# Optimization experiments

Measured on AMD Instinct MI355X. Metric: run time of the kernel, lower is better.

Reference implementation:

```python
import jax, jax.numpy as jnp
import numpy as np
import math

H = 8
D_MODEL = 512
D_K = D_MODEL // H
DIM_G = 64
WAVE_LEN = 1000.0


def box_relational_embedding(f_g):
    # f_g: [B, N, 4] -> [B, N, N, 64] trigonometric geometry embedding
    x_min, y_min, x_max, y_max = jnp.split(f_g, 4, axis=-1)  # each [B,N,1]
    cx = (x_min + x_max) * 0.5
    cy = (y_min + y_max) * 0.5
    w = x_max - x_min + 1.0
    h = y_max - y_min + 1.0
    # pairwise deltas: [B,N,1] vs [B,1,N] -> [B,N,N]
    cx_t = jnp.swapaxes(cx, 1, 2)  # [B,1,N]
    cy_t = jnp.swapaxes(cy, 1, 2)
    w_t = jnp.swapaxes(w, 1, 2)
    h_t = jnp.swapaxes(h, 1, 2)
    delta_x = jnp.log(jnp.maximum(jnp.abs((cx - cx_t) / w), 0.001))
    delta_y = jnp.log(jnp.maximum(jnp.abs((cy - cy_t) / h), 0.001))
    delta_w = jnp.log(w / w_t)
    delta_h = jnp.log(h / h_t)
    position_mat = jnp.stack([delta_x, delta_y, delta_w, delta_h], axis=-1)  # [B,N,N,4]
    feat_range = jnp.arange(DIM_G // 8, dtype=position_mat.dtype) / (DIM_G / 8)
    dim_mat = 1.0 / jnp.power(jnp.asarray(WAVE_LEN, position_mat.dtype), feat_range)  # [8]
    mul_mat = (100.0 * position_mat)[..., None] * dim_mat  # [B,N,N,4,8]
    B, N = position_mat.shape[0], position_mat.shape[1]
    mul_mat = mul_mat.reshape(B, N, N, -1)  # [B,N,N,32]
    return jnp.concatenate([jnp.sin(mul_mat), jnp.cos(mul_mat)], axis=-1)  # [B,N,N,64]


def setup_inputs() -> dict:
    key = jax.random.key(0)
    ks = jax.random.split(key, 16)
    B, N = 16, 256
    scale = 1.0 / math.sqrt(D_MODEL)
    inp = {
        'input_query': jax.random.normal(ks[0], (B, N, D_MODEL), jnp.float32),
        'input_key': jax.random.normal(ks[1], (B, N, D_MODEL), jnp.float32),
        'input_value': jax.random.normal(ks[2], (B, N, D_MODEL), jnp.float32),
        'input_box': jax.random.uniform(ks[3], (B, N, 4), jnp.float32),
        'mask': jnp.ones((B, N), jnp.int32),
        # projection weights stored as [d_in, d_out] (x @ W + b)
        'Wq': jax.random.normal(ks[4], (D_MODEL, D_MODEL), jnp.float32) * scale,
        'bq': jnp.zeros((D_MODEL,), jnp.float32),
        'Wk': jax.random.normal(ks[5], (D_MODEL, D_MODEL), jnp.float32) * scale,
        'bk': jnp.zeros((D_MODEL,), jnp.float32),
        'Wv': jax.random.normal(ks[6], (D_MODEL, D_MODEL), jnp.float32) * scale,
        'bv': jnp.zeros((D_MODEL,), jnp.float32),
        'Wo': jax.random.normal(ks[7], (D_MODEL, D_MODEL), jnp.float32) * scale,
        'bo': jnp.zeros((D_MODEL,), jnp.float32),
        # 8 geometric-bias heads: Linear(64 -> 1) each, stacked -> [H, 64], [H]
        'WG_w': jax.random.normal(ks[8], (H, DIM_G), jnp.float32) * (1.0 / math.sqrt(DIM_G)),
        'WG_b': jnp.zeros((H,), jnp.float32),
    }
    return inp


def reference(input_query, input_key, input_value, input_box, mask,
              Wq, bq, Wk, bk, Wv, bv, Wo, bo, WG_w, WG_b):
    B, N, _ = input_query.shape

    def proj(x, W, b):  # [B,N,D] -> [B,H,N,d_k]
        return (x @ W + b).reshape(B, N, H, D_K).transpose(0, 2, 1, 3)

    q = proj(input_query, Wq, bq)
    k = proj(input_key, Wk, bk)
    v = proj(input_value, Wv, bv)

    geo = box_relational_embedding(input_box)  # [B,N,N,64]
    # per-head geometric weights, ReLU'd: [B,H,N,N]
    w_g = jax.nn.relu(jnp.einsum('bnmg,hg->bhnm', geo, WG_w) + WG_b[None, :, None, None])

    scaled_dot = jnp.einsum('bhqd,bhkd->bhqk', q, k) / np.sqrt(D_K).astype(q.dtype)
    # mask: [B,N] keys -> [B,1,1,N], broadcast over heads and queries
    scaled_dot = jnp.where(mask[:, None, None, :] == 0, jnp.asarray(-1e9, scaled_dot.dtype), scaled_dot)
    w_mn = jax.nn.softmax(jnp.log(jnp.maximum(w_g, 1e-6)) + scaled_dot, axis=-1)
    # dropout is identity in eval mode
    out = jnp.einsum('bhqk,bhkd->bhqd', w_mn, v)  # [B,H,N,d_k]
    out = out.transpose(0, 2, 1, 3).reshape(B, N, H * D_K)
    return out @ Wo + bo
```

## Files before the change

### kernel.cpp

```cpp
#include <hip/hip_runtime.h>
#include <hip/hip_fp16.h>
#include <math.h>

#define Bv   16
#define Nv   256
#define Dv   512
#define Hv   8
#define MNv  4096

typedef __attribute__((ext_vector_type(8))) short bf16x8;
typedef __attribute__((ext_vector_type(4))) float f32x4;
typedef __fp16 fp16x8 __attribute__((ext_vector_type(8)));
typedef __fp16 fp16x2 __attribute__((ext_vector_type(2)));

__device__ __forceinline__ unsigned short f2bf(float f) {
    unsigned u = __float_as_uint(f);
    u = u + 0x7FFFu + ((u >> 16) & 1u);
    return (unsigned short)(u >> 16);
}
__device__ __forceinline__ void gload_lds16(const void* g, void* l) {
    __builtin_amdgcn_global_load_lds(
        (const __attribute__((address_space(1))) unsigned int*)g,
        (__attribute__((address_space(3))) unsigned int*)l, 16, 0, 0);
}

__device__ __forceinline__ void fast_sincos(float x, float* s, float* c) {
    const float rev = x * 0.15915494309189535f;
    const float fr  = rev - floorf(rev);
    *s = __builtin_amdgcn_sinf(fr);
    *c = __builtin_amdgcn_cosf(fr);
}
__device__ __forceinline__ float fast_log(float x) {
    return __builtin_amdgcn_logf(x) * 0.6931471805599453f;
}
__device__ __forceinline__ float fast_exp(float x) {
    return __builtin_amdgcn_exp2f(x * 1.4426950408889634f);
}

__global__ __launch_bounds__(256) void mega1_kernel(
    const float* __restrict__ box, const int* __restrict__ mask,
    const float* __restrict__ WGw, const float* __restrict__ WGb,
    __half* __restrict__ LB,
    const float* __restrict__ xq, const float* __restrict__ xk,
    const float* __restrict__ xv, unsigned short* __restrict__ Ab,
    const float* __restrict__ Wq, const float* __restrict__ Wk,
    const float* __restrict__ Wv, const float* __restrict__ Wo,
    const float* __restrict__ bq, const float* __restrict__ bk,
    const float* __restrict__ bv, const float* __restrict__ bo,
    unsigned short* __restrict__ Wt, float* __restrict__ biasStack)
{
    __shared__ __align__(16) char smraw[64 * 65 * 4];
    const int bid = blockIdx.x;
    const int t = threadIdx.x;

    if (bid < 4096) {
        unsigned short (*Lst)[264] = (unsigned short (*)[264])smraw;
        const int q = bid & 255;
        const int b = bid >> 8;
        const int w = t >> 6, lane = t & 63;
        const int n = lane & 15;
        const int quad = lane >> 4;

        const float4 bq_ = *(const float4*)(box + (b * Nv + q) * 4);
        const float cxq = (bq_.x + bq_.z) * 0.5f;
        const float cyq = (bq_.y + bq_.w) * 0.5f;
        const float wq  = bq_.z - bq_.x + 1.0f;
        const float hq  = bq_.w - bq_.y + 1.0f;

        union F16x8 { fp16x8 v; fp16x2 p[4]; };
        F16x8 Bs_, Bc_;
        Bs_.v = (fp16x8){}; Bc_.v = (fp16x8){};
        float bias_n = 0.0f;
        if (n < Hv) {
            bias_n = WGb[n];
#pragma unroll
            for (int jj = 0; jj < 4; ++jj) {
                Bs_.p[jj] = __builtin_amdgcn_cvt_pkrtz(WGw[n * 64 + quad * 8 + 2 * jj],
                                                       WGw[n * 64 + quad * 8 + 2 * jj + 1]);
                Bc_.p[jj] = __builtin_amdgcn_cvt_pkrtz(WGw[n * 64 + 32 + quad * 8 + 2 * jj],
                                                       WGw[n * 64 + 32 + quad * 8 + 2 * jj + 1]);
            }
        }

        const float dimm[8] = {1.0f, 0.42169650342f, 0.17782794100f, 0.07498942093f,
                               0.03162277660f, 0.01333521432f, 0.00562341325f, 0.00237137371f};
        const bool isCtr = (quad < 2);
        const bool isY   = (quad & 1);
        const float cq  = isY ? cyq : cxq;
        const float sq_ = isY ? hq : wq;

#pragma unroll
        for (int i = 0; i < 4; ++i) {
            const int m0 = (w * 4 + i) * 16;
            const float4 bm = *(const float4*)(box + (b * Nv + m0 + n) * 4);
            const float cxm = (bm.x + bm.z) * 0.5f;
            const float cym = (bm.y + bm.w) * 0.5f;
            const float wm  = bm.z - bm.x + 1.0f;
            const float hm  = bm.w - bm.y + 1.0f;
            const float cm_ = isY ? cym : cxm;
            const float sm_ = isY ? hm : wm;
            const float top = isCtr ? fabsf(cq - cm_) : sq_;
            const float bot = isCtr ? sq_ : sm_;
            float r = top * __builtin_amdgcn_rcpf(bot);
            if (isCtr) r = fmaxf(r, 1e-3f);
            const float base = 69.31471805599453f * __builtin_amdgcn_logf(r);

            float sv[8], cv[8];
#pragma unroll
            for (int j = 0; j < 8; ++j)
                fast_sincos(base * dimm[j], &sv[j], &cv[j]);

            F16x8 As_, Ac_;
#pragma unroll
            for (int jj = 0; jj < 4; ++jj) {
                As_.p[jj] = __builtin_amdgcn_cvt_pkrtz(sv[2 * jj], sv[2 * jj + 1]);
                Ac_.p[jj] = __builtin_amdgcn_cvt_pkrtz(cv[2 * jj], cv[2 * jj + 1]);
            }

            f32x4 acc = {};
            acc = __builtin_amdgcn_mfma_f32_16x16x32_f16(As_.v, Bs_.v, acc, 0, 0, 0);
            acc = __builtin_amdgcn_mfma_f32_16x16x32_f16(Ac_.v, Bc_.v, acc, 0, 0, 0);

            const int mrow = m0 + quad * 4;
            const int4 mk = *(const int4*)(mask + b * Nv + mrow);
            if (n < Hv) {
                const int* mkp = (const int*)&mk;
                const int pos0 = quad * 64 + (w * 4 + i);
#pragma unroll
                for (int rr = 0; rr < 4; ++rr) {
                    const float val = fmaxf(acc[rr] + bias_n, 1e-6f);
                    const float lb = fast_log(val) + (mkp[rr] ? 0.0f : -30000.0f);
                    Lst[n][pos0 + rr * 16] = __half_as_ushort(__float2half(lb));
                }
            }
        }

        __syncthreads();
        const int h = t >> 5, c = t & 31;
        unsigned short* dst = (unsigned short*)LB +
                              ((size_t)(b * Hv + h) * Nv + q) * Nv + c * 8;
        *(int4*)dst = *(const int4*)&Lst[h][c * 8];

    } else if (bid < 10240) {
        const int i = bid - 4096;
        const int z = i >> 11;
        const int xblk = i & 2047;
        const float* src = (z == 0) ? xq : (z == 1) ? xk : xv;
        const size_t base = (size_t)z * (MNv * Dv);
        const int idx = (xblk * 256 + t) * 4;
        float4 x = *(const float4*)(src + idx);
        ushort4 h4;
        h4.x = f2bf(x.x); h4.y = f2bf(x.y); h4.z = f2bf(x.z); h4.w = f2bf(x.w);
        *(ushort4*)(Ab + base + idx) = h4;

    } else {
        float (*T)[65] = (float (*)[65])smraw;
        const int i = bid - 10240;
        const int z = i >> 6;
        const int rem = i & 63;
        const int n0 = (rem & 7) * 64, k0 = (rem >> 3) * 64;
        const float* W = (z == 0) ? Wq : (z == 1) ? Wk : (z == 2) ? Wv : Wo;
        const float* b = (z == 0) ? bq : (z == 1) ? bk : (z == 2) ? bv : bo;
        const int col = t & 63, rb = t >> 6;
#pragma unroll
        for (int j = 0; j < 16; ++j) {
            const int row = j * 4 + rb;
            T[row][col] = W[(k0 + row) * Dv + n0 + col];
        }
        __syncthreads();
#pragma unroll
        for (int j = 0; j < 16; ++j) {
            const int row = j * 4 + rb;
            Wt[z * (Dv * Dv) + (n0 + row) * Dv + k0 + col] = f2bf(T[col][row]);
        }
        if (rem == 0) {
            biasStack[z * Dv + t]       = b[t];
            biasStack[z * Dv + t + 256] = b[t + 256];
        }
    }
}

__global__ __launch_bounds__(256) void qkv_gemm_kernel(
    const unsigned short* __restrict__ Ab, const unsigned short* __restrict__ Wt,
    const float* __restrict__ bst, unsigned short* __restrict__ Qb2,
    unsigned short* __restrict__ Kb2, unsigned short* __restrict__ Vt2)
{
    const int z = blockIdx.z;
    const unsigned short* A = Ab + (size_t)z * (MNv * Dv);
    const unsigned short* Wz = Wt + (size_t)z * (Dv * Dv);
    const float* bias = bst + z * Dv;

    const int n0 = blockIdx.x * 64;
    const int m0 = blockIdx.y * 128;
    const int t = threadIdx.x;
    const int w = t >> 6, lane = t & 63;
    const int wm = w & 1, wn = w >> 1;

    __shared__ unsigned short As[128][32];
    __shared__ unsigned short Bs[64][32];

    f32x4 acc[4][2] = {};

    const int sr = lane >> 2;
    const int sk = (lane & 3) * 8;
    const int fr = lane & 15;
    const int fk = (lane >> 4) * 8;

    for (int k0 = 0; k0 < Dv; k0 += 32) {
        __syncthreads();
#pragma unroll
        for (int j = 0; j < 2; ++j) {
            const int row = w * 32 + j * 16 + sr;
            gload_lds16(A + (size_t)(m0 + row) * Dv + k0 + sk, &As[w * 32 + j * 16][0]);
        }
        gload_lds16(Wz + (size_t)(n0 + w * 16 + sr) * Dv + k0 + sk, &Bs[w * 16][0]);
        __syncthreads();

        bf16x8 af[4], bfr[2];
#pragma unroll
        for (int mt = 0; mt < 4; ++mt)
            af[mt] = *(const bf16x8*)&As[wm * 64 + mt * 16 + fr][fk];
#pragma unroll
        for (int nt = 0; nt < 2; ++nt)
            bfr[nt] = *(const bf16x8*)&Bs[wn * 32 + nt * 16 + fr][fk];
#pragma unroll
        for (int mt = 0; mt < 4; ++mt)
#pragma unroll
            for (int nt = 0; nt < 2; ++nt)
                acc[mt][nt] = __builtin_amdgcn_mfma_f32_16x16x32_bf16(
                    af[mt], bfr[nt], acc[mt][nt], 0, 0, 0);
    }

    const int er = (lane >> 4) * 4;
    const int ec = lane & 15;
    const float scale = (z == 0) ? 0.125f : 1.0f;
#pragma unroll
    for (int nt = 0; nt < 2; ++nt) {
        const int gn = n0 + wn * 32 + nt * 16 + ec;
        const float bv_ = bias[gn];
#pragma unroll
        for (int mt = 0; mt < 4; ++mt) {
            const int gm = m0 + wm * 64 + mt * 16 + er;
            if (z == 2) {
                ushort4 o;
                o.x = f2bf(acc[mt][nt][0] + bv_);
                o.y = f2bf(acc[mt][nt][1] + bv_);
                o.z = f2bf(acc[mt][nt][2] + bv_);
                o.w = f2bf(acc[mt][nt][3] + bv_);
                *(ushort4*)(Vt2 + ((size_t)(gm >> 8) * Dv + gn) * Nv + (gm & 255)) = o;
            } else {
                unsigned short* cp = ((z == 0) ? Qb2 : Kb2) + (size_t)gm * Dv + gn;
#pragma unroll
                for (int r = 0; r < 4; ++r)
                    cp[(size_t)r * Dv] = f2bf((acc[mt][nt][r] + bv_) * scale);
            }
        }
    }
}

__global__ __launch_bounds__(256) void out_gemm_kernel(
    const unsigned short* __restrict__ A, const unsigned short* __restrict__ Wz,
    const float* __restrict__ bias, float* __restrict__ C)
{
    const int n0 = blockIdx.x * 64;
    const int m0 = blockIdx.y * 128;
    const int t = threadIdx.x;
    const int w = t >> 6, lane = t & 63;
    const int wm = w & 1, wn = w >> 1;

    __shared__ unsigned short As[128][32];
    __shared__ unsigned short Bs[64][32];

    f32x4 acc[4][2] = {};

    const int sr = lane >> 2;
    const int sk = (lane & 3) * 8;
    const int fr = lane & 15;
    const int fk = (lane >> 4) * 8;

    for (int k0 = 0; k0 < Dv; k0 += 32) {
        __syncthreads();
#pragma unroll
        for (int j = 0; j < 2; ++j) {
            const int row = w * 32 + j * 16 + sr;
            gload_lds16(A + (size_t)(m0 + row) * Dv + k0 + sk, &As[w * 32 + j * 16][0]);
        }
        gload_lds16(Wz + (size_t)(n0 + w * 16 + sr) * Dv + k0 + sk, &Bs[w * 16][0]);
        __syncthreads();

        bf16x8 af[4], bfr[2];
#pragma unroll
        for (int mt = 0; mt < 4; ++mt)
            af[mt] = *(const bf16x8*)&As[wm * 64 + mt * 16 + fr][fk];
#pragma unroll
        for (int nt = 0; nt < 2; ++nt)
            bfr[nt] = *(const bf16x8*)&Bs[wn * 32 + nt * 16 + fr][fk];
#pragma unroll
        for (int mt = 0; mt < 4; ++mt)
#pragma unroll
            for (int nt = 0; nt < 2; ++nt)
                acc[mt][nt] = __builtin_amdgcn_mfma_f32_16x16x32_bf16(
                    af[mt], bfr[nt], acc[mt][nt], 0, 0, 0);
    }

    const int er = (lane >> 4) * 4;
    const int ec = lane & 15;
#pragma unroll
    for (int nt = 0; nt < 2; ++nt) {
        const int gn = n0 + wn * 32 + nt * 16 + ec;
        const float bv_ = bias[gn];
#pragma unroll
        for (int mt = 0; mt < 4; ++mt) {
            const int gm = m0 + wm * 64 + mt * 16 + er;
            float* cp = C + (size_t)gm * Dv + gn;
#pragma unroll
            for (int r = 0; r < 4; ++r)
                cp[(size_t)r * Dv] = acc[mt][nt][r] + bv_;
        }
    }
}

__global__ __launch_bounds__(256) void attn3_kernel(
    const unsigned short* __restrict__ Qb2, const unsigned short* __restrict__ Kb2,
    const unsigned short* __restrict__ Vt2, const __half* __restrict__ LB,
    unsigned short* __restrict__ CTXb)
{
    const int qt = blockIdx.x, h = blockIdx.y, b = blockIdx.z;
    const int q0 = qt * 64;
    const int t = threadIdx.x, w = t >> 6, lane = t & 63;
    const int fr = lane & 15, fq = lane >> 4;

    __shared__ unsigned short Qs[64][72];
    __shared__ unsigned short Ks[256][72];
    __shared__ unsigned short Vt[64][264];
    unsigned short (*Pb)[264] = (unsigned short (*)[264])&Ks[0][0];

#pragma unroll
    for (int i = 0; i < 2; ++i) {
        const int idx = t + i * 256;
        const int row = idx >> 3, cu = idx & 7;
        *(bf16x8*)&Qs[row][cu * 8] =
            *(const bf16x8*)(Qb2 + (size_t)(b * Nv + q0 + row) * Dv + h * 64 + cu * 8);
    }
#pragma unroll
    for (int i = 0; i < 8; ++i) {
        const int idx = t + i * 256;
        const int row = idx >> 3, cu = idx & 7;
        *(bf16x8*)&Ks[row][cu * 8] =
            *(const bf16x8*)(Kb2 + (size_t)(b * Nv + row) * Dv + h * 64 + cu * 8);
    }
#pragma unroll
    for (int i = 0; i < 8; ++i) {
        const int idx = t + i * 256;
        const int row = idx >> 5, cu = idx & 31;
        *(bf16x8*)&Vt[row][cu * 8] =
            *(const bf16x8*)(Vt2 + (size_t)b * (Dv * Nv) + (h * 64 + row) * Nv + cu * 8);
    }

    f32x4 acc[16];
    const int qb = q0 + w * 16 + fq * 4;
    const __half* lbp = LB + ((size_t)(b * Hv + h) * Nv + qb) * Nv + fr * 16;
#pragma unroll
    for (int r = 0; r < 4; ++r) {
        union { int4 v; __half hs[8]; } u0, u1;
        const int4* p = (const int4*)(lbp + (size_t)r * Nv);
        u0.v = p[0]; u1.v = p[1];
#pragma unroll
        for (int nt = 0; nt < 8; ++nt) acc[nt][r]     = __half2float(u0.hs[nt]);
#pragma unroll
        for (int nt = 0; nt < 8; ++nt) acc[nt + 8][r] = __half2float(u1.hs[nt]);
    }

    __syncthreads();

    const bf16x8 aq0 = *(const bf16x8*)&Qs[w * 16 + fr][fq * 8];
    const bf16x8 aq1 = *(const bf16x8*)&Qs[w * 16 + fr][32 + fq * 8];
#pragma unroll
    for (int nt = 0; nt < 16; ++nt) {
        const bf16x8 bk0 = *(const bf16x8*)&Ks[nt * 16 + fr][fq * 8];
        const bf16x8 bk1 = *(const bf16x8*)&Ks[nt * 16 + fr][32 + fq * 8];
        acc[nt] = __builtin_amdgcn_mfma_f32_16x16x32_bf16(aq0, bk0, acc[nt], 0, 0, 0);
        acc[nt] = __builtin_amdgcn_mfma_f32_16x16x32_bf16(aq1, bk1, acc[nt], 0, 0, 0);
    }

    float ri[4];
#pragma unroll
    for (int r = 0; r < 4; ++r) {
        float mx = acc[0][r];
#pragma unroll
        for (int nt = 1; nt < 16; ++nt) mx = fmaxf(mx, acc[nt][r]);
        mx = fmaxf(mx, __shfl_xor(mx, 1));
        mx = fmaxf(mx, __shfl_xor(mx, 2));
        mx = fmaxf(mx, __shfl_xor(mx, 4));
        mx = fmaxf(mx, __shfl_xor(mx, 8));
        float s = 0.0f;
#pragma unroll
        for (int nt = 0; nt < 16; ++nt) {
            const float e = fast_exp(acc[nt][r] - mx);
            acc[nt][r] = e;
            s += e;
        }
        s += __shfl_xor(s, 1);
        s += __shfl_xor(s, 2);
        s += __shfl_xor(s, 4);
        s += __shfl_xor(s, 8);
        ri[r] = __builtin_amdgcn_rcpf(s);
    }

    __syncthreads();

#pragma unroll
    for (int nt = 0; nt < 16; ++nt)
#pragma unroll
        for (int r = 0; r < 4; ++r)
            Pb[w * 16 + fq * 4 + r][nt * 16 + fr] = f2bf(acc[nt][r] * ri[r]);

    f32x4 o[4] = {};
#pragma unroll
    for (int kt = 0; kt < 8; ++kt) {
        const bf16x8 ap = *(const bf16x8*)&Pb[w * 16 + fr][kt * 32 + fq * 8];
#pragma unroll
        for (int nt2 = 0; nt2 < 4; ++nt2) {
            const bf16x8 bv_ = *(const bf16x8*)&Vt[nt2 * 16 + fr][kt * 32 + fq * 8];
            o[nt2] = __builtin_amdgcn_mfma_f32_16x16x32_bf16(ap, bv_, o[nt2], 0, 0, 0);
        }
    }

#pragma unroll
    for (int nt2 = 0; nt2 < 4; ++nt2)
#pragma unroll
        for (int r = 0; r < 4; ++r)
            CTXb[(size_t)(b * Nv + qb + r) * Dv + h * 64 + nt2 * 16 + fr] =
                f2bf(o[nt2][r]);
}

extern "C" void kernel_launch(void* const* d_in, const int* in_sizes, int n_in,
                              void* d_out, int out_size, void* d_ws, size_t ws_size,
                              hipStream_t stream) {
    (void)in_sizes; (void)n_in; (void)out_size; (void)ws_size;

    const float* inq  = (const float*)d_in[0];
    const float* ink  = (const float*)d_in[1];
    const float* inv  = (const float*)d_in[2];
    const float* box  = (const float*)d_in[3];
    const int*   mask = (const int*)d_in[4];
    const float* Wq   = (const float*)d_in[5];
    const float* bq   = (const float*)d_in[6];
    const float* Wk   = (const float*)d_in[7];
    const float* bk   = (const float*)d_in[8];
    const float* Wv   = (const float*)d_in[9];
    const float* bv   = (const float*)d_in[10];
    const float* Wo   = (const float*)d_in[11];
    const float* bo   = (const float*)d_in[12];
    const float* WGw  = (const float*)d_in[13];
    const float* WGb  = (const float*)d_in[14];

    char* W = (char*)d_ws;
    const size_t MB = 1048576;
    unsigned short* Qb2  = (unsigned short*)(W + 0);
    unsigned short* Kb2  = (unsigned short*)(W + 4 * MB);
    unsigned short* Vt2  = (unsigned short*)(W + 8 * MB);
    unsigned short* Wt   = (unsigned short*)(W + 12 * MB);
    float*          bst  = (float*)(W + 14 * MB);
    unsigned short* CTXb = (unsigned short*)(W + 15 * MB);
    unsigned short* Ab   = (unsigned short*)(W + 20 * MB);
    __half*         LB   = (__half*)(W + 32 * MB);

    float* out = (float*)d_out;

    mega1_kernel<<<10496, 256, 0, stream>>>(
        box, mask, WGw, WGb, LB,
        inq, ink, inv, Ab,
        Wq, Wk, Wv, Wo, bq, bk, bv, bo, Wt, bst);

    qkv_gemm_kernel<<<dim3(8, 32, 3), 256, 0, stream>>>(Ab, Wt, bst, Qb2, Kb2, Vt2);

    attn3_kernel<<<dim3(4, 8, 16), 256, 0, stream>>>(Qb2, Kb2, Vt2, LB, CTXb);

    out_gemm_kernel<<<dim3(8, 32), 256, 0, stream>>>(CTXb, Wt + 3 * (Dv * Dv), bst + 3 * Dv, out);
}
```

Before: 157.8 us.

## Co-schedule geometry bias blocks with QKV GEMM blocks in one launch

The conversion work (activation and weight casts to bf16) now runs in its own first kernel. The geometry log-bias computation is merged into the QKV projection GEMM launch instead, with GEMM blocks interleaved one in every six block IDs. The intent is for the memory- and transcendental-heavy geometry blocks to overlap with the MFMA-bound GEMM blocks on the same CUs, filling idle units and removing the tail of separate launches. The risk is that the combined kernel's register and LDS footprint is set by the larger branch, which can lower occupancy, and that the interleaving ratio may not balance the two workloads.

New measurement: 162.2 us. +2.8%, slower.

```diff
diff --git a/kernel.cpp b/kernel.cpp
--- a/kernel.cpp
+++ b/kernel.cpp
@@ -37,10 +37,7 @@
     return __builtin_amdgcn_exp2f(x * 1.4426950408889634f);
 }
 
-__global__ __launch_bounds__(256) void mega1_kernel(
-    const float* __restrict__ box, const int* __restrict__ mask,
-    const float* __restrict__ WGw, const float* __restrict__ WGb,
-    __half* __restrict__ LB,
+__global__ __launch_bounds__(256) void conv_kernel(
     const float* __restrict__ xq, const float* __restrict__ xk,
     const float* __restrict__ xv, unsigned short* __restrict__ Ab,
     const float* __restrict__ Wq, const float* __restrict__ Wk,
@@ -49,14 +46,71 @@
     const float* __restrict__ bv, const float* __restrict__ bo,
     unsigned short* __restrict__ Wt, float* __restrict__ biasStack)
 {
-    __shared__ __align__(16) char smraw[64 * 65 * 4];
+    __shared__ float T[64][65];
     const int bid = blockIdx.x;
     const int t = threadIdx.x;
 
-    if (bid < 4096) {
+    if (bid < 6144) {
+        const int z = bid >> 11;
+        const int xblk = bid & 2047;
+        const float* src = (z == 0) ? xq : (z == 1) ? xk : xv;
+        const size_t base = (size_t)z * (MNv * Dv);
+        const int idx = (xblk * 256 + t) * 4;
+        float4 x = *(const float4*)(src + idx);
+        ushort4 h4;
+        h4.x = f2bf(x.x); h4.y = f2bf(x.y); h4.z = f2bf(x.z); h4.w = f2bf(x.w);
+        *(ushort4*)(Ab + base + idx) = h4;
+    } else {
+        const int i = bid - 6144;
+        const int z = i >> 6;
+        const int rem = i & 63;
+        const int n0 = (rem & 7) * 64, k0 = (rem >> 3) * 64;
+        const float* W = (z == 0) ? Wq : (z == 1) ? Wk : (z == 2) ? Wv : Wo;
+        const float* b = (z == 0) ? bq : (z == 1) ? bk : (z == 2) ? bv : bo;
+        const int col = t & 63, rb = t >> 6;
+#pragma unroll
+        for (int j = 0; j < 16; ++j) {
+            const int row = j * 4 + rb;
+            T[row][col] = W[(k0 + row) * Dv + n0 + col];
+        }
+        __syncthreads();
+#pragma unroll
+        for (int j = 0; j < 16; ++j) {
+            const int row = j * 4 + rb;
+            Wt[z * (Dv * Dv) + (n0 + row) * Dv + k0 + col] = f2bf(T[col][row]);
+        }
+        if (rem == 0) {
+            biasStack[z * Dv + t]       = b[t];
+            biasStack[z * Dv + t + 256] = b[t + 256];
+        }
+    }
+}
+
+__global__ __launch_bounds__(256) void geoqkv_kernel(
+    const float* __restrict__ box, const int* __restrict__ mask,
+    const float* __restrict__ WGw, const float* __restrict__ WGb,
+    __half* __restrict__ LB,
+    const unsigned short* __restrict__ Ab, const unsigned short* __restrict__ Wt,
+    const float* __restrict__ bst, unsigned short* __restrict__ Qb2,
+    unsigned short* __restrict__ Kb2, unsigned short* __restrict__ Vt2)
+{
+    __shared__ __align__(16) char smraw[12288];
+    const int bid = blockIdx.x;
+    const int t = threadIdx.x;
+
+    bool isQkv = false;
+    int ridx;
+    if (bid < 4608) {
+        if ((bid % 6) == 5) { isQkv = true; ridx = bid / 6; }
+        else                { ridx = bid - bid / 6; }
+    } else {
+        ridx = bid - 768;
+    }
+
+    if (!isQkv) {
         unsigned short (*Lst)[264] = (unsigned short (*)[264])smraw;
-        const int q = bid & 255;
-        const int b = bid >> 8;
+        const int q = ridx & 255;
+        const int b = ridx >> 8;
         const int w = t >> 6, lane = t & 63;
         const int n = lane & 15;
         const int quad = lane >> 4;
@@ -141,118 +195,77 @@
                               ((size_t)(b * Hv + h) * Nv + q) * Nv + c * 8;
         *(int4*)dst = *(const int4*)&Lst[h][c * 8];
 
-    } else if (bid < 10240) {
-        const int i = bid - 4096;
-        const int z = i >> 11;
-        const int xblk = i & 2047;
-        const float* src = (z == 0) ? xq : (z == 1) ? xk : xv;
-        const size_t base = (size_t)z * (MNv * Dv);
-        const int idx = (xblk * 256 + t) * 4;
-        float4 x = *(const float4*)(src + idx);
-        ushort4 h4;
-        h4.x = f2bf(x.x); h4.y = f2bf(x.y); h4.z = f2bf(x.z); h4.w = f2bf(x.w);
-        *(ushort4*)(Ab + base + idx) = h4;
-
     } else {
-        float (*T)[65] = (float (*)[65])smraw;
-        const int i = bid - 10240;
-        const int z = i >> 6;
-        const int rem = i & 63;
-        const int n0 = (rem & 7) * 64, k0 = (rem >> 3) * 64;
-        const float* W = (z == 0) ? Wq : (z == 1) ? Wk : (z == 2) ? Wv : Wo;
-        const float* b = (z == 0) ? bq : (z == 1) ? bk : (z == 2) ? bv : bo;
-        const int col = t & 63, rb = t >> 6;
-#pragma unroll
-        for (int j = 0; j < 16; ++j) {
-            const int row = j * 4 + rb;
-            T[row][col] = W[(k0 + row) * Dv + n0 + col];
-        }
-        __syncthreads();
-#pragma unroll
-        for (int j = 0; j < 16; ++j) {
-            const int row = j * 4 + rb;
-            Wt[z * (Dv * Dv) + (n0 + row) * Dv + k0 + col] = f2bf(T[col][row]);
-        }
-        if (rem == 0) {
-            biasStack[z * Dv + t]       = b[t];
-            biasStack[z * Dv + t + 256] = b[t + 256];
-        }
-    }
-}
-
-__global__ __launch_bounds__(256) void qkv_gemm_kernel(
-    const unsigned short* __restrict__ Ab, const unsigned short* __restrict__ Wt,
-    const float* __restrict__ bst, unsigned short* __restrict__ Qb2,
-    unsigned short* __restrict__ Kb2, unsigned short* __restrict__ Vt2)
-{
-    const int z = blockIdx.z;
-    const unsigned short* A = Ab + (size_t)z * (MNv * Dv);
-    const unsigned short* Wz = Wt + (size_t)z * (Dv * Dv);
-    const float* bias = bst + z * Dv;
-
-    const int n0 = blockIdx.x * 64;
-    const int m0 = blockIdx.y * 128;
-    const int t = threadIdx.x;
-    const int w = t >> 6, lane = t & 63;
-    const int wm = w & 1, wn = w >> 1;
-
-    __shared__ unsigned short As[128][32];
-    __shared__ unsigned short Bs[64][32];
-
-    f32x4 acc[4][2] = {};
-
-    const int sr = lane >> 2;
-    const int sk = (lane & 3) * 8;
-    const int fr = lane & 15;
-    const int fk = (lane >> 4) * 8;
-
-    for (int k0 = 0; k0 < Dv; k0 += 32) {
-        __syncthreads();
-#pragma unroll
-        for (int j = 0; j < 2; ++j) {
-            const int row = w * 32 + j * 16 + sr;
-            gload_lds16(A + (size_t)(m0 + row) * Dv + k0 + sk, &As[w * 32 + j * 16][0]);
-        }
-        gload_lds16(Wz + (size_t)(n0 + w * 16 + sr) * Dv + k0 + sk, &Bs[w * 16][0]);
-        __syncthreads();
-
-        bf16x8 af[4], bfr[2];
-#pragma unroll
-        for (int mt = 0; mt < 4; ++mt)
-            af[mt] = *(const bf16x8*)&As[wm * 64 + mt * 16 + fr][fk];
-#pragma unroll
-        for (int nt = 0; nt < 2; ++nt)
-            bfr[nt] = *(const bf16x8*)&Bs[wn * 32 + nt * 16 + fr][fk];
-#pragma unroll
-        for (int mt = 0; mt < 4; ++mt)
+        unsigned short (*As)[32] = (unsigned short (*)[32])smraw;
+        unsigned short (*Bs)[32] = (unsigned short (*)[32])(smraw + 8192);
+
+        const int z = ridx >> 8;
+        const int rem = ridx & 255;
+        const int n0 = (rem & 7) * 64;
+        const int m0 = (rem >> 3) * 128;
+
+        const unsigned short* A = Ab + (size_t)z * (MNv * Dv);
+        const unsigned short* Wz = Wt + (size_t)z * (Dv * Dv);
+        const float* bias = bst + z * Dv;
+
+        const int w = t >> 6, lane = t & 63;
+        const int wm = w & 1, wn = w >> 1;
+
+        f32x4 acc[4][2] = {};
+
+        const int sr = lane >> 2;
+        const int sk = (lane & 3) * 8;
+        const int fr = lane & 15;
+        const int fk = (lane >> 4) * 8;
+
+        for (int k0 = 0; k0 < Dv; k0 += 32) {
+            __syncthreads();
+#pragma unroll
+            for (int j = 0; j < 2; ++j) {
+                const int row = w * 32 + j * 16 + sr;
+                gload_lds16(A + (size_t)(m0 + row) * Dv + k0 + sk, &As[w * 32 + j * 16][0]);
+            }
+            gload_lds16(Wz + (size_t)(n0 + w * 16 + sr) * Dv + k0 + sk, &Bs[w * 16][0]);
+            __syncthreads();
+
+            bf16x8 af[4], bfr[2];
+#pragma unroll
+            for (int mt = 0; mt < 4; ++mt)
+                af[mt] = *(const bf16x8*)&As[wm * 64 + mt * 16 + fr][fk];
 #pragma unroll
             for (int nt = 0; nt < 2; ++nt)
-                acc[mt][nt] = __builtin_amdgcn_mfma_f32_16x16x32_bf16(
-                    af[mt], bfr[nt], acc[mt][nt], 0, 0, 0);
-    }
-
-    const int er = (lane >> 4) * 4;
-    const int ec = lane & 15;
-    const float scale = (z == 0) ? 0.125f : 1.0f;
-#pragma unroll
-    for (int nt = 0; nt < 2; ++nt) {
-        const int gn = n0 + wn * 32 + nt * 16 + ec;
-        const float bv_ = bias[gn];
-#pragma unroll
-        for (int mt = 0; mt < 4; ++mt) {
-            const int gm = m0 + wm * 64 + mt * 16 + er;
-            if (z == 2) {
-                ushort4 o;
-                o.x = f2bf(acc[mt][nt][0] + bv_);
-                o.y = f2bf(acc[mt][nt][1] + bv_);
-                o.z = f2bf(acc[mt][nt][2] + bv_);
-                o.w = f2bf(acc[mt][nt][3] + bv_);
-                *(ushort4*)(Vt2 + ((size_t)(gm >> 8) * Dv + gn) * Nv + (gm & 255)) = o;
-            } else {
-                unsigned short* cp = ((z == 0) ? Qb2 : Kb2) + (size_t)gm * Dv + gn;
-#pragma unroll
-                for (int r = 0; r < 4; ++r)
-                    cp[(size_t)r * Dv] = f2bf((acc[mt][nt][r] + bv_) * scale);
+                bfr[nt] = *(const bf16x8*)&Bs[wn * 32 + nt * 16 + fr][fk];
+#pragma unroll
+            for (int mt = 0; mt < 4; ++mt)
+#pragma unroll
+                for (int nt = 0; nt < 2; ++nt)
+                    acc[mt][nt] = __builtin_amdgcn_mfma_f32_16x16x32_bf16(
+                        af[mt], bfr[nt], acc[mt][nt], 0, 0, 0);
+        }
+
+        const int er = (lane >> 4) * 4;
+        const int ec = lane & 15;
+        const float scale = (z == 0) ? 0.125f : 1.0f;
+#pragma unroll
+        for (int nt = 0; nt < 2; ++nt) {
+            const int gn = n0 + wn * 32 + nt * 16 + ec;
+            const float bv_ = bias[gn];
+#pragma unroll
+            for (int mt = 0; mt < 4; ++mt) {
+                const int gm = m0 + wm * 64 + mt * 16 + er;
+                if (z == 2) {
+                    ushort4 o;
+                    o.x = f2bf(acc[mt][nt][0] + bv_);
+                    o.y = f2bf(acc[mt][nt][1] + bv_);
+                    o.z = f2bf(acc[mt][nt][2] + bv_);
+                    o.w = f2bf(acc[mt][nt][3] + bv_);
+                    *(ushort4*)(Vt2 + ((size_t)(gm >> 8) * Dv + gn) * Nv + (gm & 255)) = o;
+                } else {
+                    unsigned short* cp = ((z == 0) ? Qb2 : Kb2) + (size_t)gm * Dv + gn;
+#pragma unroll
+                    for (int r = 0; r < 4; ++r)
+                        cp[(size_t)r * Dv] = f2bf((acc[mt][nt][r] + bv_) * scale);
+                }
             }
         }
     }
@@ -468,12 +481,11 @@
 
     float* out = (float*)d_out;
 
-    mega1_kernel<<<10496, 256, 0, stream>>>(
-        box, mask, WGw, WGb, LB,
-        inq, ink, inv, Ab,
-        Wq, Wk, Wv, Wo, bq, bk, bv, bo, Wt, bst);
-
-    qkv_gemm_kernel<<<dim3(8, 32, 3), 256, 0, stream>>>(Ab, Wt, bst, Qb2, Kb2, Vt2);
+    conv_kernel<<<6400, 256, 0, stream>>>(
+        inq, ink, inv, Ab, Wq, Wk, Wv, Wo, bq, bk, bv, bo, Wt, bst);
+
+    geoqkv_kernel<<<4864, 256, 0, stream>>>(
+        box, mask, WGw, WGb, LB, Ab, Wt, bst, Qb2, Kb2, Vt2);
 
     attn3_kernel<<<dim3(4, 8, 16), 256, 0, stream>>>(Qb2, Kb2, Vt2, LB, CTXb);
 
```

## Fuse fp32-to-half input conversion into QKV GEMM and switch pipeline to fp16

Applied to the files above, without the earlier changes.

Drops the separate pass in the first kernel that converted the query, key and value inputs to bf16 through a workspace buffer. The QKV GEMM now reads fp32 activations directly, converts them to fp16 in registers and stores them into shared memory. All matmuls switch from bf16 to fp16 MFMA, with weights and intermediates stored as fp16. This removes one full write and reread of the activations, but A-tile loads become synchronous register loads instead of direct global-to-LDS copies, and fp16's narrower range could overflow on large values.

Measured after the change: 166.9 us. 1.06x slower.

```diff
diff --git a/kernel.cpp b/kernel.cpp
--- a/kernel.cpp
+++ b/kernel.cpp
@@ -8,16 +8,10 @@
 #define Hv   8
 #define MNv  4096
 
-typedef __attribute__((ext_vector_type(8))) short bf16x8;
 typedef __attribute__((ext_vector_type(4))) float f32x4;
 typedef __fp16 fp16x8 __attribute__((ext_vector_type(8)));
 typedef __fp16 fp16x2 __attribute__((ext_vector_type(2)));
 
-__device__ __forceinline__ unsigned short f2bf(float f) {
-    unsigned u = __float_as_uint(f);
-    u = u + 0x7FFFu + ((u >> 16) & 1u);
-    return (unsigned short)(u >> 16);
-}
 __device__ __forceinline__ void gload_lds16(const void* g, void* l) {
     __builtin_amdgcn_global_load_lds(
         (const __attribute__((address_space(1))) unsigned int*)g,
@@ -36,13 +30,14 @@
 __device__ __forceinline__ float fast_exp(float x) {
     return __builtin_amdgcn_exp2f(x * 1.4426950408889634f);
 }
+__device__ __forceinline__ unsigned short f2h(float x) {
+    return __half_as_ushort(__float2half(x));
+}
 
 __global__ __launch_bounds__(256) void mega1_kernel(
     const float* __restrict__ box, const int* __restrict__ mask,
     const float* __restrict__ WGw, const float* __restrict__ WGb,
     __half* __restrict__ LB,
-    const float* __restrict__ xq, const float* __restrict__ xk,
-    const float* __restrict__ xv, unsigned short* __restrict__ Ab,
     const float* __restrict__ Wq, const float* __restrict__ Wk,
     const float* __restrict__ Wv, const float* __restrict__ Wo,
     const float* __restrict__ bq, const float* __restrict__ bk,
@@ -130,7 +125,7 @@
                 for (int rr = 0; rr < 4; ++rr) {
                     const float val = fmaxf(acc[rr] + bias_n, 1e-6f);
                     const float lb = fast_log(val) + (mkp[rr] ? 0.0f : -30000.0f);
-                    Lst[n][pos0 + rr * 16] = __half_as_ushort(__float2half(lb));
+                    Lst[n][pos0 + rr * 16] = f2h(lb);
                 }
             }
         }
@@ -141,21 +136,9 @@
                               ((size_t)(b * Hv + h) * Nv + q) * Nv + c * 8;
         *(int4*)dst = *(const int4*)&Lst[h][c * 8];
 
-    } else if (bid < 10240) {
-        const int i = bid - 4096;
-        const int z = i >> 11;
-        const int xblk = i & 2047;
-        const float* src = (z == 0) ? xq : (z == 1) ? xk : xv;
-        const size_t base = (size_t)z * (MNv * Dv);
-        const int idx = (xblk * 256 + t) * 4;
-        float4 x = *(const float4*)(src + idx);
-        ushort4 h4;
-        h4.x = f2bf(x.x); h4.y = f2bf(x.y); h4.z = f2bf(x.z); h4.w = f2bf(x.w);
-        *(ushort4*)(Ab + base + idx) = h4;
-
     } else {
         float (*T)[65] = (float (*)[65])smraw;
-        const int i = bid - 10240;
+        const int i = bid - 4096;
         const int z = i >> 6;
         const int rem = i & 63;
         const int n0 = (rem & 7) * 64, k0 = (rem >> 3) * 64;
@@ -171,7 +154,7 @@
 #pragma unroll
         for (int j = 0; j < 16; ++j) {
             const int row = j * 4 + rb;
-            Wt[z * (Dv * Dv) + (n0 + row) * Dv + k0 + col] = f2bf(T[col][row]);
+            Wt[z * (Dv * Dv) + (n0 + row) * Dv + k0 + col] = f2h(T[col][row]);
         }
         if (rem == 0) {
             biasStack[z * Dv + t]       = b[t];
@@ -181,12 +164,13 @@
 }
 
 __global__ __launch_bounds__(256) void qkv_gemm_kernel(
-    const unsigned short* __restrict__ Ab, const unsigned short* __restrict__ Wt,
+    const float* __restrict__ xq, const float* __restrict__ xk,
+    const float* __restrict__ xv, const unsigned short* __restrict__ Wt,
     const float* __restrict__ bst, unsigned short* __restrict__ Qb2,
     unsigned short* __restrict__ Kb2, unsigned short* __restrict__ Vt2)
 {
     const int z = blockIdx.z;
-    const unsigned short* A = Ab + (size_t)z * (MNv * Dv);
+    const float* A = (z == 0) ? xq : (z == 1) ? xk : xv;
     const unsigned short* Wz = Wt + (size_t)z * (Dv * Dv);
     const float* bias = bst + z * Dv;
 
@@ -201,33 +185,48 @@
 
     f32x4 acc[4][2] = {};
 
+    const int arow = t >> 1;
+    const int ahalf = (t & 1) * 16;
     const int sr = lane >> 2;
     const int sk = (lane & 3) * 8;
     const int fr = lane & 15;
     const int fk = (lane >> 4) * 8;
 
+    union V16 { fp16x2 p[4]; int4 v; };
+
     for (int k0 = 0; k0 < Dv; k0 += 32) {
-        __syncthreads();
-#pragma unroll
-        for (int j = 0; j < 2; ++j) {
-            const int row = w * 32 + j * 16 + sr;
-            gload_lds16(A + (size_t)(m0 + row) * Dv + k0 + sk, &As[w * 32 + j * 16][0]);
-        }
+        const float* ap = A + (size_t)(m0 + arow) * Dv + k0 + ahalf;
+        const float4 a0 = *(const float4*)(ap);
+        const float4 a1 = *(const float4*)(ap + 4);
+        const float4 a2 = *(const float4*)(ap + 8);
+        const float4 a3 = *(const float4*)(ap + 12);
+        __syncthreads();
         gload_lds16(Wz + (size_t)(n0 + w * 16 + sr) * Dv + k0 + sk, &Bs[w * 16][0]);
-        __syncthreads();
-
-        bf16x8 af[4], bfr[2];
+        V16 u0, u1;
+        u0.p[0] = __builtin_amdgcn_cvt_pkrtz(a0.x, a0.y);
+        u0.p[1] = __builtin_amdgcn_cvt_pkrtz(a0.z, a0.w);
+        u0.p[2] = __builtin_amdgcn_cvt_pkrtz(a1.x, a1.y);
+        u0.p[3] = __builtin_amdgcn_cvt_pkrtz(a1.z, a1.w);
+        u1.p[0] = __builtin_amdgcn_cvt_pkrtz(a2.x, a2.y);
+        u1.p[1] = __builtin_amdgcn_cvt_pkrtz(a2.z, a2.w);
+        u1.p[2] = __builtin_amdgcn_cvt_pkrtz(a3.x, a3.y);
+        u1.p[3] = __builtin_amdgcn_cvt_pkrtz(a3.z, a3.w);
+        *(int4*)&As[arow][ahalf]     = u0.v;
+        *(int4*)&As[arow][ahalf + 8] = u1.v;
+        __syncthreads();
+
+        fp16x8 af[4], bfr[2];
 #pragma unroll
         for (int mt = 0; mt < 4; ++mt)
-            af[mt] = *(const bf16x8*)&As[wm * 64 + mt * 16 + fr][fk];
+            af[mt] = *(const fp16x8*)&As[wm * 64 + mt * 16 + fr][fk];
 #pragma unroll
         for (int nt = 0; nt < 2; ++nt)
-            bfr[nt] = *(const bf16x8*)&Bs[wn * 32 + nt * 16 + fr][fk];
+            bfr[nt] = *(const fp16x8*)&Bs[wn * 32 + nt * 16 + fr][fk];
 #pragma unroll
         for (int mt = 0; mt < 4; ++mt)
 #pragma unroll
             for (int nt = 0; nt < 2; ++nt)
-                acc[mt][nt] = __builtin_amdgcn_mfma_f32_16x16x32_bf16(
+                acc[mt][nt] = __builtin_amdgcn_mfma_f32_16x16x32_f16(
                     af[mt], bfr[nt], acc[mt][nt], 0, 0, 0);
     }
 
@@ -242,17 +241,17 @@
         for (int mt = 0; mt < 4; ++mt) {
             const int gm = m0 + wm * 64 + mt * 16 + er;
             if (z == 2) {
-                ushort4 o;
-                o.x = f2bf(acc[mt][nt][0] + bv_);
-                o.y = f2bf(acc[mt][nt][1] + bv_);
-                o.z = f2bf(acc[mt][nt][2] + bv_);
-                o.w = f2bf(acc[mt][nt][3] + bv_);
-                *(ushort4*)(Vt2 + ((size_t)(gm >> 8) * Dv + gn) * Nv + (gm & 255)) = o;
+                union { fp16x2 p[2]; ushort4 u; } o;
+                o.p[0] = __builtin_amdgcn_cvt_pkrtz(acc[mt][nt][0] + bv_,
+                                                    acc[mt][nt][1] + bv_);
+                o.p[1] = __builtin_amdgcn_cvt_pkrtz(acc[mt][nt][2] + bv_,
+                                                    acc[mt][nt][3] + bv_);
+                *(ushort4*)(Vt2 + ((size_t)(gm >> 8) * Dv + gn) * Nv + (gm & 255)) = o.u;
             } else {
                 unsigned short* cp = ((z == 0) ? Qb2 : Kb2) + (size_t)gm * Dv + gn;
 #pragma unroll
                 for (int r = 0; r < 4; ++r)
-                    cp[(size_t)r * Dv] = f2bf((acc[mt][nt][r] + bv_) * scale);
+                    cp[(size_t)r * Dv] = f2h((acc[mt][nt][r] + bv_) * scale);
             }
         }
     }
@@ -288,18 +287,18 @@
         gload_lds16(Wz + (size_t)(n0 + w * 16 + sr) * Dv + k0 + sk, &Bs[w * 16][0]);
         __syncthreads();
 
-        bf16x8 af[4], bfr[2];
+        fp16x8 af[4], bfr[2];
 #pragma unroll
         for (int mt = 0; mt < 4; ++mt)
-            af[mt] = *(const bf16x8*)&As[wm * 64 + mt * 16 + fr][fk];
+            af[mt] = *(const fp16x8*)&As[wm * 64 + mt * 16 + fr][fk];
 #pragma unroll
         for (int nt = 0; nt < 2; ++nt)
-            bfr[nt] = *(const bf16x8*)&Bs[wn * 32 + nt * 16 + fr][fk];
+            bfr[nt] = *(const fp16x8*)&Bs[wn * 32 + nt * 16 + fr][fk];
 #pragma unroll
         for (int mt = 0; mt < 4; ++mt)
 #pragma unroll
             for (int nt = 0; nt < 2; ++nt)
-                acc[mt][nt] = __builtin_amdgcn_mfma_f32_16x16x32_bf16(
+                acc[mt][nt] = __builtin_amdgcn_mfma_f32_16x16x32_f16(
                     af[mt], bfr[nt], acc[mt][nt], 0, 0, 0);
     }
 
@@ -323,7 +322,7 @@
 __global__ __launch_bounds__(256) void attn3_kernel(
     const unsigned short* __restrict__ Qb2, const unsigned short* __restrict__ Kb2,
     const unsigned short* __restrict__ Vt2, const __half* __restrict__ LB,
-    unsigned short* __restrict__ CTXb)
+    unsigned short* __restrict__ CTXh)
 {
     const int qt = blockIdx.x, h = blockIdx.y, b = blockIdx.z;
     const int q0 = qt * 64;
@@ -339,22 +338,22 @@
     for (int i = 0; i < 2; ++i) {
         const int idx = t + i * 256;
         const int row = idx >> 3, cu = idx & 7;
-        *(bf16x8*)&Qs[row][cu * 8] =
-            *(const bf16x8*)(Qb2 + (size_t)(b * Nv + q0 + row) * Dv + h * 64 + cu * 8);
+        *(int4*)&Qs[row][cu * 8] =
+            *(const int4*)(Qb2 + (size_t)(b * Nv + q0 + row) * Dv + h * 64 + cu * 8);
     }
 #pragma unroll
     for (int i = 0; i < 8; ++i) {
         const int idx = t + i * 256;
         const int row = idx >> 3, cu = idx & 7;
-        *(bf16x8*)&Ks[row][cu * 8] =
-            *(const bf16x8*)(Kb2 + (size_t)(b * Nv + row) * Dv + h * 64 + cu * 8);
+        *(int4*)&Ks[row][cu * 8] =
+            *(const int4*)(Kb2 + (size_t)(b * Nv + row) * Dv + h * 64 + cu * 8);
     }
 #pragma unroll
     for (int i = 0; i < 8; ++i) {
         const int idx = t + i * 256;
         const int row = idx >> 5, cu = idx & 31;
-        *(bf16x8*)&Vt[row][cu * 8] =
-            *(const bf16x8*)(Vt2 + (size_t)b * (Dv * Nv) + (h * 64 + row) * Nv + cu * 8);
+        *(int4*)&Vt[row][cu * 8] =
+            *(const int4*)(Vt2 + (size_t)b * (Dv * Nv) + (h * 64 + row) * Nv + cu * 8);
     }
 
     f32x4 acc[16];
@@ -373,14 +372,14 @@
 
     __syncthreads();
 
-    const bf16x8 aq0 = *(const bf16x8*)&Qs[w * 16 + fr][fq * 8];
-    const bf16x8 aq1 = *(const bf16x8*)&Qs[w * 16 + fr][32 + fq * 8];
+    const fp16x8 aq0 = *(const fp16x8*)&Qs[w * 16 + fr][fq * 8];
+    const fp16x8 aq1 = *(const fp16x8*)&Qs[w * 16 + fr][32 + fq * 8];
 #pragma unroll
     for (int nt = 0; nt < 16; ++nt) {
-        const bf16x8 bk0 = *(const bf16x8*)&Ks[nt * 16 + fr][fq * 8];
-        const bf16x8 bk1 = *(const bf16x8*)&Ks[nt * 16 + fr][32 + fq * 8];
-        acc[nt] = __builtin_amdgcn_mfma_f32_16x16x32_bf16(aq0, bk0, acc[nt], 0, 0, 0);
-        acc[nt] = __builtin_amdgcn_mfma_f32_16x16x32_bf16(aq1, bk1, acc[nt], 0, 0, 0);
+        const fp16x8 bk0 = *(const fp16x8*)&Ks[nt * 16 + fr][fq * 8];
+        const fp16x8 bk1 = *(const fp16x8*)&Ks[nt * 16 + fr][32 + fq * 8];
+        acc[nt] = __builtin_amdgcn_mfma_f32_16x16x32_f16(aq0, bk0, acc[nt], 0, 0, 0);
+        acc[nt] = __builtin_amdgcn_mfma_f32_16x16x32_f16(aq1, bk1, acc[nt], 0, 0, 0);
     }
 
     float ri[4];
@@ -413,16 +412,16 @@
     for (int nt = 0; nt < 16; ++nt)
 #pragma unroll
         for (int r = 0; r < 4; ++r)
-            Pb[w * 16 + fq * 4 + r][nt * 16 + fr] = f2bf(acc[nt][r] * ri[r]);
+            Pb[w * 16 + fq * 4 + r][nt * 16 + fr] = f2h(acc[nt][r] * ri[r]);
 
     f32x4 o[4] = {};
 #pragma unroll
     for (int kt = 0; kt < 8; ++kt) {
-        const bf16x8 ap = *(const bf16x8*)&Pb[w * 16 + fr][kt * 32 + fq * 8];
+        const fp16x8 ap = *(const fp16x8*)&Pb[w * 16 + fr][kt * 32 + fq * 8];
 #pragma unroll
         for (int nt2 = 0; nt2 < 4; ++nt2) {
-            const bf16x8 bv_ = *(const bf16x8*)&Vt[nt2 * 16 + fr][kt * 32 + fq * 8];
-            o[nt2] = __builtin_amdgcn_mfma_f32_16x16x32_bf16(ap, bv_, o[nt2], 0, 0, 0);
+            const fp16x8 bv_ = *(const fp16x8*)&Vt[nt2 * 16 + fr][kt * 32 + fq * 8];
+            o[nt2] = __builtin_amdgcn_mfma_f32_16x16x32_f16(ap, bv_, o[nt2], 0, 0, 0);
         }
     }
 
@@ -430,8 +429,8 @@
     for (int nt2 = 0; nt2 < 4; ++nt2)
 #pragma unroll
         for (int r = 0; r < 4; ++r)
-            CTXb[(size_t)(b * Nv + qb + r) * Dv + h * 64 + nt2 * 16 + fr] =
-                f2bf(o[nt2][r]);
+            CTXh[(size_t)(b * Nv + qb + r) * Dv + h * 64 + nt2 * 16 + fr] =
+                f2h(o[nt2][r]);
 }
 
 extern "C" void kernel_launch(void* const* d_in, const int* in_sizes, int n_in,
@@ -462,20 +461,19 @@
     unsigned short* Vt2  = (unsigned short*)(W + 8 * MB);
     unsigned short* Wt   = (unsigned short*)(W + 12 * MB);
     float*          bst  = (float*)(W + 14 * MB);
-    unsigned short* CTXb = (unsigned short*)(W + 15 * MB);
-    unsigned short* Ab   = (unsigned short*)(W + 20 * MB);
-    __half*         LB   = (__half*)(W + 32 * MB);
+    unsigned short* CTXh = (unsigned short*)(W + 15 * MB);
+    __half*         LB   = (__half*)(W + 20 * MB);
 
     float* out = (float*)d_out;
 
-    mega1_kernel<<<10496, 256, 0, stream>>>(
+    mega1_kernel<<<4352, 256, 0, stream>>>(
         box, mask, WGw, WGb, LB,
-        inq, ink, inv, Ab,
         Wq, Wk, Wv, Wo, bq, bk, bv, bo, Wt, bst);
 
-    qkv_gemm_kernel<<<dim3(8, 32, 3), 256, 0, stream>>>(Ab, Wt, bst, Qb2, Kb2, Vt2);
-
-    attn3_kernel<<<dim3(4, 8, 16), 256, 0, stream>>>(Qb2, Kb2, Vt2, LB, CTXb);
-
-    out_gemm_kernel<<<dim3(8, 32), 256, 0, stream>>>(CTXb, Wt + 3 * (Dv * Dv), bst + 3 * Dv, out);
-}
+    qkv_gemm_kernel<<<dim3(8, 32, 3), 256, 0, stream>>>(
+        inq, ink, inv, Wt, bst, Qb2, Kb2, Vt2);
+
+    attn3_kernel<<<dim3(4, 8, 16), 256, 0, stream>>>(Qb2, Kb2, Vt2, LB, CTXh);
+
+    out_gemm_kernel<<<dim3(8, 32), 256, 0, stream>>>(CTXh, Wt + 3 * (Dv * Dv), bst + 3 * Dv, out);
+}
```
